# Kernel tuning notes

Measured on AMD Instinct MI355X. Metric: run time of the kernel, lower is better.

Reference implementation:

```python
import jax, jax.numpy as jnp
import numpy as np

H, KVH, D = 8, 4, 256
SCALING = 256.0 ** -0.5   # query_pre_attn_scalar ** -0.5
SOFTCAP = 50.0
THETA = 10000.0
WINDOW = 1024


def setup_inputs() -> dict:
    key = jax.random.key(0)
    ks = jax.random.split(key, 5)
    B, S, HID = 2, 2048, 2304
    return {
        "hidden_states": jax.random.normal(ks[0], (B, S, HID), jnp.float32),
        "Wq": jax.random.normal(ks[1], (H * D, HID), jnp.float32) * 0.02,
        "Wk": jax.random.normal(ks[2], (KVH * D, HID), jnp.float32) * 0.02,
        "Wv": jax.random.normal(ks[3], (KVH * D, HID), jnp.float32) * 0.02,
        "Wo": jax.random.normal(ks[4], (HID, H * D), jnp.float32) * 0.02,
        "position_ids": jnp.arange(S, dtype=jnp.int32),
    }


def _rotate_half(x):
    x1, x2 = x[..., : D // 2], x[..., D // 2 :]
    return jnp.concatenate((-x2, x1), axis=-1)


def reference(hidden_states, Wq, Wk, Wv, Wo, position_ids):
    B, S, HID = hidden_states.shape
    # projections (torch Linear: y = x @ W.T)
    q = (hidden_states @ Wq.T).reshape(B, S, H, D).transpose(0, 2, 1, 3)      # [B,H,S,D]
    k = (hidden_states @ Wk.T).reshape(B, S, KVH, D).transpose(0, 2, 1, 3)    # [B,KVH,S,D]
    v = (hidden_states @ Wv.T).reshape(B, S, KVH, D).transpose(0, 2, 1, 3)

    # rotary embedding
    inv_freq = 1.0 / (THETA ** (jnp.arange(0, D, 2, dtype=jnp.float32) / D))  # [D/2]
    freqs = position_ids.astype(jnp.float32)[:, None] * inv_freq[None, :]     # [S,D/2]
    emb = jnp.concatenate((freqs, freqs), axis=-1)                            # [S,D]
    cos = jnp.cos(emb)[None, None]                                            # [1,1,S,D]
    sin = jnp.sin(emb)[None, None]
    q = q * cos + _rotate_half(q) * sin
    k = k * cos + _rotate_half(k) * sin

    # repeat_kv (GQA)
    n_rep = H // KVH
    k = jnp.repeat(k, n_rep, axis=1)  # [B,H,S,D]
    v = jnp.repeat(v, n_rep, axis=1)

    # softcapped attention scores
    scores = jnp.einsum("bhqd,bhkd->bhqk", q, k) * SCALING
    scores = SOFTCAP * jnp.tanh(scores / SOFTCAP)

    # causal + sliding-window mask
    i = jnp.arange(S)[:, None]
    j = jnp.arange(S)[None, :]
    allowed = (j <= i) & (i - j < WINDOW)
    scores = jnp.where(allowed[None, None], scores, jnp.finfo(scores.dtype).min)

    attn = jax.nn.softmax(scores.astype(jnp.float32), axis=-1).astype(q.dtype)
    out = jnp.einsum("bhqk,bhkd->bhqd", attn, v)          # [B,H,S,D]
    out = out.transpose(0, 2, 1, 3).reshape(B, S, H * D)   # [B,S,H*D]
    return out @ Wo.T                                      # [B,S,HID]
```

## Files before the change

kernel.cpp:

```cpp
#include <hip/hip_runtime.h>

typedef _Float16 half8 __attribute__((ext_vector_type(8)));
typedef _Float16 half4v __attribute__((ext_vector_type(4)));
typedef float floatx4 __attribute__((ext_vector_type(4)));
typedef float floatx16 __attribute__((ext_vector_type(16)));

#define GLD16(g, l) __builtin_amdgcn_global_load_lds(                          \
    (__attribute__((address_space(1))) void*)(g),                              \
    (__attribute__((address_space(3))) void*)(l), 16, 0, 0)

#define VM4 asm volatile("s_waitcnt vmcnt(4)" ::: "memory")
#define VM0 asm volatile("s_waitcnt vmcnt(0)" ::: "memory")

__global__ void cvt_all(const float* __restrict__ s0, const float* __restrict__ s1,
                        const float* __restrict__ s2, const float* __restrict__ s3,
                        const float* __restrict__ s4, _Float16* __restrict__ d0,
                        _Float16* __restrict__ d1, _Float16* __restrict__ d2,
                        _Float16* __restrict__ d3, _Float16* __restrict__ d4) {
  long i = (long)blockIdx.x * 256 + threadIdx.x;
  const float* s;
  _Float16* d;
  long off;
  long roff;
  if (i < 2359296) {
    s = s0; d = d0; off = i; roff = off;
  } else if (i < 3538944) {
    s = s1; d = d1; off = i - 2359296;
    const int r = (int)(off / 576), cu = (int)(off % 576);
    const int h = r >> 8, e = r & 255;
    const int srcr = (h << 8) + ((e & 1) ? (e >> 1) + 128 : (e >> 1));
    roff = (long)srcr * 576 + cu;
  } else if (i < 4128768) {
    s = s2; d = d2; off = i - 3538944;
    const int r = (int)(off / 576), cu = (int)(off % 576);
    const int h = r >> 8, e = r & 255;
    const int srcr = (h << 8) + ((e & 1) ? (e >> 1) + 128 : (e >> 1));
    roff = (long)srcr * 576 + cu;
  } else if (i < 4718592) {
    s = s3; d = d3; off = i - 4128768; roff = off;
  } else {
    s = s4; d = d4; off = i - 4718592; roff = off;
  }
  const float4 v = *(const float4*)(s + roff * 4);
  half4v o = {(_Float16)v.x, (_Float16)v.y, (_Float16)v.z, (_Float16)v.w};
  *(half4v*)(d + off * 4) = o;
}

__device__ __forceinline__ void stg_half(const _Float16* __restrict__ g,
                                         _Float16* l, int h, long k0, int K,
                                         int tid, const long* gofs) {
#pragma unroll
  for (int p = 0; p < 2; ++p)
    GLD16(g + (long)h * 128 * K + k0 + gofs[p],
          l + (h * 1024 + p * 512 + tid) * 8);
}

#define LDB(buf)                                                               \
  _Pragma("unroll") for (int n = 0; n < 4; ++n)                                \
  _Pragma("unroll") for (int ks = 0; ks < 2; ++ks)                             \
      bfr[n][ks] = *(const half8*)&lB[buf][boff0 + n * 1024 +                  \
                                           (((ks * 4 + quad) ^ xq) << 3)];

#define PH(buf, q, VMW, ...)                                                   \
  {                                                                            \
    half8 af[2][2];                                                            \
    _Pragma("unroll") for (int m2 = 0; m2 < 2; ++m2)                           \
    _Pragma("unroll") for (int ks = 0; ks < 2; ++ks)                           \
        af[m2][ks] = *(const half8*)&lA[buf][aoff0 + ((q) * 2 + m2) * 1024 +   \
                                             (((ks * 4 + quad) ^ xq) << 3)];   \
    __VA_ARGS__;                                                               \
    __builtin_amdgcn_sched_barrier(0);                                         \
    __builtin_amdgcn_s_barrier();                                              \
    __builtin_amdgcn_sched_barrier(0);                                         \
    __builtin_amdgcn_s_setprio(1);                                             \
    _Pragma("unroll") for (int ks = 0; ks < 2; ++ks)                           \
    _Pragma("unroll") for (int m2 = 0; m2 < 2; ++m2)                           \
    _Pragma("unroll") for (int n = 0; n < 4; ++n)                              \
        acc[(q) * 2 + m2][n] = __builtin_amdgcn_mfma_f32_16x16x32_f16(         \
            af[m2][ks], bfr[n][ks], acc[(q) * 2 + m2][n], 0, 0, 0);            \
    __builtin_amdgcn_s_setprio(0);                                             \
    VMW;                                                                       \
    __builtin_amdgcn_sched_barrier(0);                                         \
    __builtin_amdgcn_s_barrier();                                              \
    __builtin_amdgcn_sched_barrier(0);                                         \
  }

template <typename TO, bool ROPE>
__global__ __launch_bounds__(512, 2) void gemm256(
    const _Float16* __restrict__ A, const _Float16* __restrict__ B,
    TO* __restrict__ C, int M, int N, int K, _Float16* __restrict__ Qr,
    _Float16* __restrict__ Kr, const int* __restrict__ pos) {
  __shared__ __align__(16) _Float16 lA[2][16384];
  __shared__ __align__(16) _Float16 lB[2][16384];
  const int tid = threadIdx.x;
  const int lane = tid & 63;
  const int w = tid >> 6;
  const int wm = w >> 2, wn = w & 3;
  const int quad = lane >> 4, l15 = lane & 15;
  const int xq = l15 & 7;

  const int nwg = gridDim.x * gridDim.y;
  int wg = blockIdx.y * gridDim.x + blockIdx.x;
  if (!(nwg & 7)) wg = (wg & 7) * (nwg >> 3) + (wg >> 3);
  const int bx = wg % gridDim.x, by = wg / gridDim.x;
  const long tM = (long)by * 256, tN = (long)bx * 256;

  const _Float16* Ab = A + tM * K;
  const _Float16* Bb = B + tN * K;

  long gofs[2];
#pragma unroll
  for (int p = 0; p < 2; ++p) {
    const int U = p * 512 + tid;
    const int r = U >> 3;
    gofs[p] = (long)r * K + (((U & 7) ^ (r & 7)) << 3);
  }

  const int aoff0 = (wm * 128 + l15) * 64;
  const int boff0 = (wn * 64 + l15) * 64;

  floatx4 acc[8][4] = {};
  half8 bfr[4][2];

  stg_half(Bb, &lB[0][0], 0, 0, K, tid, gofs);
  stg_half(Bb, &lB[0][0], 1, 0, K, tid, gofs);
  stg_half(Ab, &lA[0][0], 0, 0, K, tid, gofs);
  stg_half(Ab, &lA[0][0], 1, 0, K, tid, gofs);
  stg_half(Bb, &lB[1][0], 0, 64, K, tid, gofs);
  stg_half(Bb, &lB[1][0], 1, 64, K, tid, gofs);
  VM4;
  __builtin_amdgcn_sched_barrier(0);
  __builtin_amdgcn_s_barrier();
  __builtin_amdgcn_sched_barrier(0);

  const int NI = K >> 7;
  for (int i = 0; i < NI; ++i) {
    const long ks0 = (long)i << 7;
    const bool fin = (i == NI - 1);
    LDB(0);
    PH(0, 0, (void)0, stg_half(Ab, &lA[1][0], 0, ks0 + 64, K, tid, gofs));
    PH(0, 1, (void)0, stg_half(Ab, &lA[1][0], 1, ks0 + 64, K, tid, gofs));
    PH(0, 2, (void)0,
       if (!fin) stg_half(Bb, &lB[0][0], 0, ks0 + 128, K, tid, gofs));
    PH(0, 3, if (fin) { VM0; } else { VM4; },
       if (!fin) stg_half(Bb, &lB[0][0], 1, ks0 + 128, K, tid, gofs));
    LDB(1);
    PH(1, 0, (void)0,
       if (!fin) stg_half(Ab, &lA[0][0], 0, ks0 + 128, K, tid, gofs));
    PH(1, 1, (void)0,
       if (!fin) stg_half(Ab, &lA[0][0], 1, ks0 + 128, K, tid, gofs));
    PH(1, 2, (void)0,
       if (!fin) stg_half(Bb, &lB[1][0], 0, ks0 + 192, K, tid, gofs));
    PH(1, 3, if (!fin) { VM4; },
       if (!fin) stg_half(Bb, &lB[1][0], 1, ks0 + 192, K, tid, gofs));
  }

  if constexpr (ROPE) {
    if (tN < 3072) {
      const int b = (int)(tM >> 11);
      const int s0 = (int)(tM & 2047);
      _Float16* dst0;
      if (tN < 2048)
        dst0 = Qr + (((long)b * 8 + (int)(tN >> 8)) * 2048) * 256;
      else
        dst0 = Kr + (((long)b * 4 + (int)((tN - 2048) >> 8)) * 2048) * 256;
      const int par = l15 & 1;
      float invf[4];
      int dofs[4];
#pragma unroll
      for (int n = 0; n < 4; ++n) {
        const int p = wn * 32 + n * 8 + (l15 >> 1);
        invf[n] = __expf((float)p * -0.07195578164f);
        dofs[n] = p + par * 128;
      }
#pragma unroll
      for (int m = 0; m < 8; ++m) {
#pragma unroll
        for (int r = 0; r < 4; ++r) {
          const int row = wm * 128 + m * 16 + quad * 4 + r;
          const float pv = (float)pos[s0 + row];
          _Float16* drow = dst0 + ((long)(s0 + row)) * 256;
#pragma unroll
          for (int n = 0; n < 4; ++n) {
            const float v = acc[m][n][r];
            const float px = __shfl_xor(v, 1, 64);
            float sn, cs;
            __sincosf(pv * invf[n], &sn, &cs);
            const float o = par ? (v * cs + px * sn) : (v * cs - px * sn);
            drow[dofs[n]] = (_Float16)o;
          }
        }
      }
      return;
    }
  }
#pragma unroll
  for (int m = 0; m < 8; ++m) {
#pragma unroll
    for (int n = 0; n < 4; ++n) {
      const long col = tN + wn * 64 + n * 16 + l15;
      const long row0 = tM + wm * 128 + m * 16 + quad * 4;
#pragma unroll
      for (int r = 0; r < 4; ++r)
        C[(row0 + r) * N + col] = (TO)acc[m][n][r];
    }
  }
}

__global__ void vtrans(const _Float16* __restrict__ QKV,
                       _Float16* __restrict__ Vt) {
  __shared__ _Float16 lT[64 * 65];
  const int tid = threadIdx.x;
  const int ss = blockIdx.x * 64;
  const int dd = blockIdx.y * 64;
  const int z = blockIdx.z;
  const int b = z >> 2, kvh = z & 3;

#pragma unroll
  for (int pass = 0; pass < 2; ++pass) {
    const int U = pass * 256 + tid;
    const int s_loc = U >> 3, du = U & 7;
    const half8 v = *(const half8*)(QKV + ((long)(b * 2048 + ss + s_loc)) * 4096 +
                                    3072 + kvh * 256 + dd + du * 8);
#pragma unroll
    for (int e = 0; e < 8; ++e) lT[s_loc * 65 + du * 8 + e] = v[e];
  }
  __syncthreads();
#pragma unroll
  for (int pass = 0; pass < 2; ++pass) {
    const int U = pass * 256 + tid;
    const int su = U & 7, dl = (U >> 3) & 63;
    half8 o;
#pragma unroll
    for (int e = 0; e < 8; ++e) o[e] = lT[(su * 8 + e) * 65 + dl];
    *(half8*)(Vt + ((long)z * 256 + dd + dl) * 2048 + ss + su * 8) = o;
  }
}

__global__ __launch_bounds__(256, 2) void attn_fwd(
    const _Float16* __restrict__ Q, const _Float16* __restrict__ K,
    const _Float16* __restrict__ Vt, _Float16* __restrict__ AO) {
  __shared__ __align__(16) _Float16 lK[2][64 * 256];
  __shared__ __align__(16) _Float16 lP[64 * 76];

  const int tid = threadIdx.x;
  const int lane = tid & 63;
  const int w = tid >> 6;
  const int quad = lane >> 4, l15 = lane & 15;

  const int qt = blockIdx.x;
  const int h = blockIdx.y;
  const int b = blockIdx.z;
  const int kvh = h >> 1;
  const int qs = qt * 64;

  const _Float16* Qb = Q + (((long)b * 8 + h) * 2048) * 256;
  const _Float16* Kb = K + (((long)b * 4 + kvh) * 2048) * 256;
  const _Float16* Vb = Vt + (((long)b * 4 + kvh) * 256) * 2048;

  half8 qf[8];
  {
    const _Float16* qp = Qb + (long)(qs + w * 16 + l15) * 256 + quad * 8;
#pragma unroll
    for (int t = 0; t < 8; ++t) qf[t] = *(const half8*)(qp + t * 32);
  }
  half8 onesv;
#pragma unroll
  for (int e = 0; e < 8; ++e) onesv[e] = (_Float16)1.f;

  floatx4 o[4][4] = {};
  floatx4 lacc[4] = {};

  const int kt_lo = qt >= 16 ? qt - 16 : 0;

  {
    const _Float16* kt0 = Kb + (long)kt_lo * 64 * 256;
#pragma unroll
    for (int p = 0; p < 8; ++p) {
      const int U = p * 256 + tid;
      const int r = U >> 5, u = U & 31;
      GLD16(kt0 + r * 256 + ((u ^ (r & 7)) << 3), &lK[0][U * 8]);
    }
  }

  int cur = 0;
  for (int kt = kt_lo; kt <= qt; ++kt, cur ^= 1) {
    const int ks = kt * 64;
    __syncthreads();

    half8 vf[2][4];
#pragma unroll
    for (int t2 = 0; t2 < 2; ++t2)
#pragma unroll
      for (int j = 0; j < 4; ++j) {
        const int d = w * 64 + j * 16 + l15;
        vf[t2][j] = *(const half8*)(Vb + (long)d * 2048 + ks + t2 * 32 + quad * 8);
      }
    if (kt < qt) {
      const _Float16* kt0 = Kb + (long)(ks + 64) * 256;
      const int nxt = cur ^ 1;
#pragma unroll
      for (int p = 0; p < 8; ++p) {
        const int U = p * 256 + tid;
        const int r = U >> 5, u = U & 31;
        GLD16(kt0 + r * 256 + ((u ^ (r & 7)) << 3), &lK[nxt][U * 8]);
      }
    }

    floatx4 sc[4] = {};
#pragma unroll
    for (int t = 0; t < 8; ++t)
#pragma unroll
      for (int j = 0; j < 4; ++j) {
        const half8 kf = *(const half8*)&lK[cur][(j * 16 + l15) * 256 +
                                                 (((t * 4 + quad) ^ (l15 & 7)) << 3)];
        sc[j] = __builtin_amdgcn_mfma_f32_16x16x32_f16(qf[t], kf, sc[j], 0, 0, 0);
      }

    const bool need_mask = (kt == qt) || (kt == qt - 16);
    const int qr0 = qs + w * 16 + quad * 4;
#pragma unroll
    for (int j = 0; j < 4; ++j) {
      const int key = ks + j * 16 + l15;
#pragma unroll
      for (int r = 0; r < 4; ++r) {
        const float s = sc[j][r] * 0.0625f;
        const float t2 = (s * 0.02f) * (s * 0.02f);
        const float cap = s * (1.f + t2 * (-0.33333333f + t2 * 0.13333333f));
        float p = __expf(cap - 5.f);
        if (need_mask) {
          const bool ok = (key <= qr0 + r) && (qr0 + r - key < 1024);
          p = ok ? p : 0.f;
        }
        lP[(w * 16 + quad * 4 + r) * 76 + j * 16 + l15] = (_Float16)p;
      }
    }
    __syncthreads();

#pragma unroll
    for (int t2 = 0; t2 < 2; ++t2) {
      half8 pf[4];
#pragma unroll
      for (int i = 0; i < 4; ++i)
        pf[i] = *(const half8*)&lP[(i * 16 + l15) * 76 + t2 * 32 + quad * 8];
#pragma unroll
      for (int i = 0; i < 4; ++i) {
        lacc[i] = __builtin_amdgcn_mfma_f32_16x16x32_f16(pf[i], onesv, lacc[i],
                                                         0, 0, 0);
#pragma unroll
        for (int j = 0; j < 4; ++j)
          o[i][j] = __builtin_amdgcn_mfma_f32_16x16x32_f16(pf[i], vf[t2][j],
                                                           o[i][j], 0, 0, 0);
      }
    }
  }

  _Float16* aop = AO + ((long)b * 2048 + qs) * 2048 + (long)h * 256;
#pragma unroll
  for (int i = 0; i < 4; ++i)
#pragma unroll
    for (int r = 0; r < 4; ++r) {
      const int row = i * 16 + quad * 4 + r;
      const float inv = 1.0f / lacc[i][r];
#pragma unroll
      for (int j = 0; j < 4; ++j)
        aop[(long)row * 2048 + w * 64 + j * 16 + l15] =
            (_Float16)(o[i][j][r] * inv);
    }
}

extern "C" void kernel_launch(void* const* d_in, const int* in_sizes, int n_in,
                              void* d_out, int out_size, void* d_ws,
                              size_t ws_size, hipStream_t stream) {
  const float* hs = (const float*)d_in[0];
  const float* Wq = (const float*)d_in[1];
  const float* Wk = (const float*)d_in[2];
  const float* Wv = (const float*)d_in[3];
  const float* Wo = (const float*)d_in[4];
  const int* pos = (const int*)d_in[5];
  float* out = (float*)d_out;

  _Float16* Xf = (_Float16*)d_ws;
  _Float16* Wqkv = Xf + 4096L * 2304;
  _Float16* Wo16 = Wqkv + 4096L * 2304;
  _Float16* QKV = Wo16 + 2304L * 2048;
  _Float16* Qr = QKV + 4096L * 4096;
  _Float16* Kr = Qr + 2L * 8 * 2048 * 256;
  _Float16* Vt = Kr + 2L * 4 * 2048 * 256;
  _Float16* AO = Xf;

  cvt_all<<<dim3(23040), dim3(256), 0, stream>>>(
      hs, Wq, Wk, Wv, Wo, Xf, Wqkv, Wqkv + 2048L * 2304, Wqkv + 3072L * 2304,
      Wo16);

  gemm256<_Float16, true><<<dim3(16, 16), dim3(512), 0, stream>>>(
      Xf, Wqkv, QKV, 4096, 4096, 2304, Qr, Kr, pos);
  vtrans<<<dim3(32, 4, 8), dim3(256), 0, stream>>>(QKV, Vt);
  attn_fwd<<<dim3(32, 8, 2), dim3(256), 0, stream>>>(Qr, Kr, Vt, AO);
  gemm256<float, false><<<dim3(9, 16), dim3(512), 0, stream>>>(
      AO, Wo16, out, 4096, 2304, 2048, nullptr, nullptr, nullptr);
}
```

Baseline: 331.8 us.

## Split-K the output projection GEMM with atomic accumulation into zeroed output

The output projection GEMM launched only 144 workgroups (9x16), which underfills the GPU. It is now split along K into 4 chunks of 512, giving 576 workgroups that accumulate into the fp32 output with atomicAdd. The output buffer is zeroed inside the existing conversion kernel by launching extra blocks. The cost is atomic traffic on the 4096x2304 output, results that depend on summation order, and the extra zeroing pass.

```diff
diff --git a/kernel.cpp b/kernel.cpp
--- a/kernel.cpp
+++ b/kernel.cpp
@@ -3,7 +3,6 @@
 typedef _Float16 half8 __attribute__((ext_vector_type(8)));
 typedef _Float16 half4v __attribute__((ext_vector_type(4)));
 typedef float floatx4 __attribute__((ext_vector_type(4)));
-typedef float floatx16 __attribute__((ext_vector_type(16)));
 
 #define GLD16(g, l) __builtin_amdgcn_global_load_lds(                          \
     (__attribute__((address_space(1))) void*)(g),                              \
@@ -16,12 +15,19 @@
                         const float* __restrict__ s2, const float* __restrict__ s3,
                         const float* __restrict__ s4, _Float16* __restrict__ d0,
                         _Float16* __restrict__ d1, _Float16* __restrict__ d2,
-                        _Float16* __restrict__ d3, _Float16* __restrict__ d4) {
+                        _Float16* __restrict__ d3, _Float16* __restrict__ d4,
+                        float* __restrict__ z0) {
   long i = (long)blockIdx.x * 256 + threadIdx.x;
   const float* s;
   _Float16* d;
   long off;
   long roff;
+  if (i >= 5898240) {
+    const long zo = (i - 5898240) * 4;
+    const float4 z = {0.f, 0.f, 0.f, 0.f};
+    *(float4*)(z0 + zo) = z;
+    return;
+  }
   if (i < 2359296) {
     s = s0; d = d0; off = i; roff = off;
   } else if (i < 3538944) {
@@ -85,11 +91,12 @@
     __builtin_amdgcn_sched_barrier(0);                                         \
   }
 
-template <typename TO, bool ROPE>
+template <typename TO, bool ROPE, bool SPLITK>
 __global__ __launch_bounds__(512, 2) void gemm256(
     const _Float16* __restrict__ A, const _Float16* __restrict__ B,
-    TO* __restrict__ C, int M, int N, int K, _Float16* __restrict__ Qr,
-    _Float16* __restrict__ Kr, const int* __restrict__ pos) {
+    TO* __restrict__ C, int M, int N, int K, int KC,
+    _Float16* __restrict__ Qr, _Float16* __restrict__ Kr,
+    const int* __restrict__ pos) {
   __shared__ __align__(16) _Float16 lA[2][16384];
   __shared__ __align__(16) _Float16 lB[2][16384];
   const int tid = threadIdx.x;
@@ -105,8 +112,9 @@
   const int bx = wg % gridDim.x, by = wg / gridDim.x;
   const long tM = (long)by * 256, tN = (long)bx * 256;
 
-  const _Float16* Ab = A + tM * K;
-  const _Float16* Bb = B + tN * K;
+  const long kOff = SPLITK ? (long)blockIdx.z * KC : 0;
+  const _Float16* Ab = A + tM * K + kOff;
+  const _Float16* Bb = B + tN * K + kOff;
 
   long gofs[2];
 #pragma unroll
@@ -133,7 +141,7 @@
   __builtin_amdgcn_s_barrier();
   __builtin_amdgcn_sched_barrier(0);
 
-  const int NI = K >> 7;
+  const int NI = KC >> 7;
   for (int i = 0; i < NI; ++i) {
     const long ks0 = (long)i << 7;
     const bool fin = (i == NI - 1);
@@ -201,8 +209,12 @@
       const long col = tN + wn * 64 + n * 16 + l15;
       const long row0 = tM + wm * 128 + m * 16 + quad * 4;
 #pragma unroll
-      for (int r = 0; r < 4; ++r)
-        C[(row0 + r) * N + col] = (TO)acc[m][n][r];
+      for (int r = 0; r < 4; ++r) {
+        if constexpr (SPLITK)
+          atomicAdd(&C[(row0 + r) * N + col], acc[m][n][r]);
+        else
+          C[(row0 + r) * N + col] = (TO)acc[m][n][r];
+      }
     }
   }
 }
@@ -389,14 +401,14 @@
   _Float16* Vt = Kr + 2L * 4 * 2048 * 256;
   _Float16* AO = Xf;
 
-  cvt_all<<<dim3(23040), dim3(256), 0, stream>>>(
+  cvt_all<<<dim3(32256), dim3(256), 0, stream>>>(
       hs, Wq, Wk, Wv, Wo, Xf, Wqkv, Wqkv + 2048L * 2304, Wqkv + 3072L * 2304,
-      Wo16);
-
-  gemm256<_Float16, true><<<dim3(16, 16), dim3(512), 0, stream>>>(
-      Xf, Wqkv, QKV, 4096, 4096, 2304, Qr, Kr, pos);
+      Wo16, out);
+
+  gemm256<_Float16, true, false><<<dim3(16, 16), dim3(512), 0, stream>>>(
+      Xf, Wqkv, QKV, 4096, 4096, 2304, 2304, Qr, Kr, pos);
   vtrans<<<dim3(32, 4, 8), dim3(256), 0, stream>>>(QKV, Vt);
   attn_fwd<<<dim3(32, 8, 2), dim3(256), 0, stream>>>(Qr, Kr, Vt, AO);
-  gemm256<float, false><<<dim3(9, 16), dim3(512), 0, stream>>>(
-      AO, Wo16, out, 4096, 2304, 2048, nullptr, nullptr, nullptr);
-}
+  gemm256<float, false, true><<<dim3(9, 16, 4), dim3(512), 0, stream>>>(
+      AO, Wo16, out, 4096, 2304, 2048, 512, nullptr, nullptr, nullptr);
+}
```

Measured after the change: 427.3 us. 28.8% more time.
